# Kernel tuning notes

Hardware: AMD Instinct MI355X
Metric: run time of the kernel (lower is better)

The kernel has to match this reference:

```python
import jax, jax.numpy as jnp
import numpy as np

N, B, F = 204800, 4096, 256

def setup_inputs() -> dict:
    key = jax.random.key(0)
    ks = jax.random.split(key, 8)
    s = 1.0 / np.sqrt(F)
    return {
        'node_feats': jax.random.normal(ks[0], (N, F), jnp.float32),
        'g_feats': jax.random.normal(ks[1], (B, F), jnp.float32),
        'segment_ids': jnp.sort(jax.random.randint(ks[2], (N,), 0, B, jnp.int32)),
        'W_logit': jax.random.normal(ks[3], (1, 2 * F), jnp.float32) * (1.0 / np.sqrt(2 * F)),
        'b_logit': jnp.zeros((1,), jnp.float32),
        'W_proj': jax.random.normal(ks[4], (F, F), jnp.float32) * s,
        'b_proj': jnp.zeros((F,), jnp.float32),
        'W_ih': jax.random.normal(ks[5], (3 * F, F), jnp.float32) * s,
        'W_hh': jax.random.normal(ks[6], (3 * F, F), jnp.float32) * s,
        'b_ih': jnp.zeros((3 * F,), jnp.float32),
        'b_hh': jnp.zeros((3 * F,), jnp.float32),
    }

def reference(node_feats, g_feats, segment_ids, W_logit, b_logit, W_proj, b_proj, W_ih, W_hh, b_ih, b_hh):
    num_graphs = g_feats.shape[0]
    # logits: Linear(2F -> 1) on [broadcast(relu(g_feats)), node_feats], then LeakyReLU(0.01)
    ctx_nodes = jax.nn.relu(g_feats)[segment_ids]                      # [N, F]
    z = jnp.concatenate([ctx_nodes, node_feats], axis=1) @ W_logit.T + b_logit  # [N, 1]
    z = jax.nn.leaky_relu(z, negative_slope=0.01)
    # per-graph segment softmax over nodes
    zmax = jax.ops.segment_max(z, segment_ids, num_segments=num_graphs)
    z_exp = jnp.exp(z - zmax[segment_ids])
    denom = jax.ops.segment_sum(z_exp, segment_ids, num_segments=num_graphs)
    a = z_exp / denom[segment_ids]                                     # [N, 1]
    # project nodes (Dropout is identity at eval) and weighted segment sum
    hv = node_feats @ W_proj.T + b_proj                                # [N, F]
    g_repr = jax.ops.segment_sum(a * hv, segment_ids, num_segments=num_graphs)  # [B, F]
    context = jax.nn.elu(g_repr)
    # PyTorch GRUCell: input=context, hidden=g_feats
    gi = context @ W_ih.T + b_ih                                       # [B, 3F]
    gh = g_feats @ W_hh.T + b_hh
    i_r, i_z, i_n = jnp.split(gi, 3, axis=1)
    h_r, h_z, h_n = jnp.split(gh, 3, axis=1)
    r = jax.nn.sigmoid(i_r + h_r)
    zg = jax.nn.sigmoid(i_z + h_z)
    n = jnp.tanh(i_n + r * h_n)
    return (1.0 - zg) * n + zg * g_feats
```

## Files before the change

kernel.cpp:

```cpp
#include <hip/hip_runtime.h>

#define NN 204800
#define BB 4096
#define FF 256

typedef unsigned short u16;
typedef unsigned int u32;
typedef short bf16x8 __attribute__((ext_vector_type(8)));
typedef float f32x4  __attribute__((ext_vector_type(4)));

__device__ __forceinline__ u16 rne_bf16(float f){
    union { u32 v; float f; } t; t.f = f;
    u32 lsb = (t.v >> 16) & 1u;
    t.v += 0x7fffu + lsb;
    return (u16)(t.v >> 16);
}

__global__ void k_prep(const float* __restrict__ gfe, const float* __restrict__ Wp,
                       const float* __restrict__ Wih, const float* __restrict__ Whh,
                       const int* __restrict__ seg, int* __restrict__ start,
                       u16* __restrict__ gfe_b, u16* __restrict__ Wp_b,
                       u16* __restrict__ Wih_b, u16* __restrict__ Whh_b){
    int i = blockIdx.x * 256 + threadIdx.x;
    if (i <= BB){
        int lo = 0, hi = NN;
        while (lo < hi){ int mid = (lo + hi) >> 1; if (seg[mid] < i) lo = mid + 1; else hi = mid; }
        start[i] = lo;
    }
    const int n_gfe = BB * FF;
    const int n_wp  = FF * FF;
    const int n_w3  = 3 * FF * FF;
    int j = i;
    if (j < n_gfe){ gfe_b[j] = rne_bf16(gfe[j]); return; }
    j -= n_gfe;
    if (j < n_wp){ Wp_b[j] = rne_bf16(Wp[j]); return; }
    j -= n_wp;
    if (j < n_w3){ Wih_b[j] = rne_bf16(Wih[j]); return; }
    j -= n_w3;
    if (j < n_w3){ Whh_b[j] = rne_bf16(Whh[j]); return; }
}
#define PREP_TOTAL (BB*FF + FF*FF + 2*3*FF*FF)

__global__ void k_ctx_logit(const float* __restrict__ gfe, const float* __restrict__ Wl,
                            const float* __restrict__ bl, float* __restrict__ c){
    int wave = threadIdx.x >> 6, lane = threadIdx.x & 63;
    int g = blockIdx.x * 4 + wave;
    float4 gv = *(const float4*)(gfe + (size_t)g * FF + lane * 4);
    float4 wv = *(const float4*)(Wl + lane * 4);
    float sum = wv.x * fmaxf(gv.x, 0.f) + wv.y * fmaxf(gv.y, 0.f)
              + wv.z * fmaxf(gv.z, 0.f) + wv.w * fmaxf(gv.w, 0.f);
    #pragma unroll
    for (int o = 32; o; o >>= 1) sum += __shfl_xor(sum, o);
    if (lane == 0) c[g] = sum + bl[0];
}

__global__ void k_node_logit(const float* __restrict__ x, const float* __restrict__ Wl,
                             const float* __restrict__ c, const int* __restrict__ seg,
                             float* __restrict__ z){
    int wave = threadIdx.x >> 6, lane = threadIdx.x & 63;
    int n = blockIdx.x * 4 + wave;
    float4 xv = *(const float4*)(x + (size_t)n * FF + lane * 4);
    float4 wv = *(const float4*)(Wl + FF + lane * 4);
    float sum = xv.x * wv.x + xv.y * wv.y + xv.z * wv.z + xv.w * wv.w;
    #pragma unroll
    for (int o = 32; o; o >>= 1) sum += __shfl_xor(sum, o);
    if (lane == 0){
        float t = c[seg[n]] + sum;
        z[n] = t >= 0.f ? t : 0.01f * t;
    }
}

__global__ void k_stats(const float* __restrict__ z, const int* __restrict__ start,
                        float* __restrict__ m, float* __restrict__ invd){
    int wave = threadIdx.x >> 6, lane = threadIdx.x & 63;
    int g = blockIdx.x * 4 + wave;
    if (g >= BB) return;
    int s0 = start[g], s1 = start[g + 1];
    float mx = -3.4e38f;
    for (int i = s0 + lane; i < s1; i += 64) mx = fmaxf(mx, z[i]);
    #pragma unroll
    for (int o = 32; o; o >>= 1) mx = fmaxf(mx, __shfl_xor(mx, o));
    float d = 0.f;
    for (int i = s0 + lane; i < s1; i += 64) d += expf(z[i] - mx);
    #pragma unroll
    for (int o = 32; o; o >>= 1) d += __shfl_xor(d, o);
    if (lane == 0){
        m[g] = mx;
        invd[g] = (s1 > s0) ? (1.f / d) : 0.f;
    }
}

__global__ void k_wsum(const float* __restrict__ x, const float* __restrict__ z,
                       const int* __restrict__ start, const float* __restrict__ m,
                       const float* __restrict__ invd, u16* __restrict__ s_b){
    int g = blockIdx.x;
    int t = threadIdx.x;
    int s0 = start[g], s1 = start[g + 1];
    float mg = m[g], iv = invd[g];
    float acc = 0.f;
    for (int n = s0; n < s1; n++){
        float w = expf(z[n] - mg);
        acc += w * x[(size_t)n * FF + t];
    }
    s_b[(size_t)g * FF + t] = rne_bf16(acc * iv);
}

__global__ __launch_bounds__(256) void k_proj_mfma(
        const u16* __restrict__ s_b, const u16* __restrict__ Wp_b,
        const float* __restrict__ bp, const int* __restrict__ gate,
        u16* __restrict__ ctx_b){
    int tid = threadIdx.x;
    int w = tid >> 6, l = tid & 63;
    int mn = l & 15, q = l >> 4;
    int m0 = blockIdx.x * 64 + w * 16;
    int f0 = blockIdx.y * 64;
    f32x4 acc[4] = {};
    const u16* arow = s_b + (size_t)(m0 + mn) * FF + q * 8;
    #pragma unroll
    for (int kb = 0; kb < 8; kb++){
        bf16x8 a = *(const bf16x8*)(arow + kb * 32);
        #pragma unroll
        for (int c = 0; c < 4; c++){
            bf16x8 b = *(const bf16x8*)(Wp_b + (size_t)(f0 + c * 16 + mn) * FF + kb * 32 + q * 8);
            acc[c] = __builtin_amdgcn_mfma_f32_16x16x32_bf16(a, b, acc[c], 0, 0, 0);
        }
    }
    #pragma unroll
    for (int c = 0; c < 4; c++){
        int f = f0 + c * 16 + mn;
        float bias = bp[f];
        #pragma unroll
        for (int r = 0; r < 4; r++){
            int g = m0 + q * 4 + r;
            float bs = (gate[g + 1] > gate[g]) ? 1.f : 0.f;
            float v = acc[c][r] + bs * bias;
            v = v > 0.f ? v : expm1f(v);
            ctx_b[(size_t)g * FF + f] = rne_bf16(v);
        }
    }
}

__global__ __launch_bounds__(256) void k_gru_mfma(
        const u16* __restrict__ ctx_b, const u16* __restrict__ gfe_b,
        const u16* __restrict__ Wih_b, const u16* __restrict__ Whh_b,
        const float* __restrict__ bih, const float* __restrict__ bhh,
        const float* __restrict__ gfe, float* __restrict__ out){
    int tid = threadIdx.x;
    int w = tid >> 6, l = tid & 63;
    int mn = l & 15, q = l >> 4;
    int g0 = blockIdx.x * 64 + w * 16;
    int f0 = blockIdx.y * 64;
    f32x4 ai[3][4] = {};
    f32x4 ah[3][4] = {};
    const u16* ac_row = ctx_b + (size_t)(g0 + mn) * FF + q * 8;
    const u16* ag_row = gfe_b + (size_t)(g0 + mn) * FF + q * 8;
    #pragma unroll
    for (int kb = 0; kb < 8; kb++){
        bf16x8 a_c = *(const bf16x8*)(ac_row + kb * 32);
        bf16x8 a_g = *(const bf16x8*)(ag_row + kb * 32);
        #pragma unroll
        for (int s = 0; s < 3; s++){
            #pragma unroll
            for (int c = 0; c < 4; c++){
                size_t woff = (size_t)(s * FF + f0 + c * 16 + mn) * FF + kb * 32 + q * 8;
                bf16x8 bi = *(const bf16x8*)(Wih_b + woff);
                ai[s][c] = __builtin_amdgcn_mfma_f32_16x16x32_bf16(a_c, bi, ai[s][c], 0, 0, 0);
                bf16x8 bh = *(const bf16x8*)(Whh_b + woff);
                ah[s][c] = __builtin_amdgcn_mfma_f32_16x16x32_bf16(a_g, bh, ah[s][c], 0, 0, 0);
            }
        }
    }
    #pragma unroll
    for (int c = 0; c < 4; c++){
        int f = f0 + c * 16 + mn;
        float bir = bih[f], biz = bih[FF + f], bin_ = bih[2 * FF + f];
        float bhr = bhh[f], bhz = bhh[FF + f], bhn = bhh[2 * FF + f];
        #pragma unroll
        for (int r = 0; r < 4; r++){
            int g = g0 + q * 4 + r;
            float rg = 1.f / (1.f + expf(-(ai[0][c][r] + bir + ah[0][c][r] + bhr)));
            float zg = 1.f / (1.f + expf(-(ai[1][c][r] + biz + ah[1][c][r] + bhz)));
            float ng = tanhf(ai[2][c][r] + bin_ + rg * (ah[2][c][r] + bhn));
            float h = gfe[(size_t)g * FF + f];
            out[(size_t)g * FF + f] = (1.f - zg) * ng + zg * h;
        }
    }
}

extern "C" void kernel_launch(void* const* d_in, const int* in_sizes, int n_in,
                              void* d_out, int out_size, void* d_ws, size_t ws_size,
                              hipStream_t stream){
    const float* node = (const float*)d_in[0];
    const float* gfe  = (const float*)d_in[1];
    const int*   seg  = (const int*)d_in[2];
    const float* Wl   = (const float*)d_in[3];
    const float* bl   = (const float*)d_in[4];
    const float* Wp   = (const float*)d_in[5];
    const float* bp   = (const float*)d_in[6];
    const float* Wih  = (const float*)d_in[7];
    const float* Whh  = (const float*)d_in[8];
    const float* bih  = (const float*)d_in[9];
    const float* bhh  = (const float*)d_in[10];
    float* out = (float*)d_out;

    char* p = (char*)d_ws;
    auto alloc = [&](size_t bytes)->void*{
        void* r = (void*)p; p += (bytes + 255) & ~(size_t)255; return r;
    };
    int*   start = (int*)  alloc((BB + 1) * sizeof(int));
    float* c     = (float*)alloc(BB * sizeof(float));
    float* z     = (float*)alloc(NN * sizeof(float));
    float* mbuf  = (float*)alloc(BB * sizeof(float));
    float* invd  = (float*)alloc(BB * sizeof(float));
    u16*   s_b   = (u16*)  alloc((size_t)BB * FF * sizeof(u16));
    u16*   ctx_b = (u16*)  alloc((size_t)BB * FF * sizeof(u16));
    u16*   gfe_b = (u16*)  alloc((size_t)BB * FF * sizeof(u16));
    u16*   Wp_b  = (u16*)  alloc((size_t)FF * FF * sizeof(u16));
    u16*   Wih_b = (u16*)  alloc((size_t)3 * FF * FF * sizeof(u16));
    u16*   Whh_b = (u16*)  alloc((size_t)3 * FF * FF * sizeof(u16));

    k_prep<<<(PREP_TOTAL + 255) / 256, 256, 0, stream>>>(gfe, Wp, Wih, Whh, seg, start,
                                                         gfe_b, Wp_b, Wih_b, Whh_b);
    k_ctx_logit<<<BB / 4, 256, 0, stream>>>(gfe, Wl, bl, c);
    k_node_logit<<<NN / 4, 256, 0, stream>>>(node, Wl, c, seg, z);
    k_stats<<<BB / 4, 256, 0, stream>>>(z, start, mbuf, invd);
    k_wsum<<<BB, 256, 0, stream>>>(node, z, start, mbuf, invd, s_b);
    k_proj_mfma<<<dim3(BB / 64, FF / 64), 256, 0, stream>>>(s_b, Wp_b, bp, start, ctx_b);
    k_gru_mfma<<<dim3(BB / 64, FF / 64), 256, 0, stream>>>(ctx_b, gfe_b, Wih_b, Whh_b,
                                                           bih, bhh, gfe, out);
}
```

Baseline: 409.9 us.

## Fuse node logits, segment softmax and weighted sum into one per-graph kernel

Replaces three kernels (node logits, per-segment max/denominator, weighted node sum) with a single kernel that runs one block per graph. Each block computes the node logits and stages up to 64 node rows in shared memory, then does the softmax and the weighted sum from that copy. This avoids a second global read of node_feats, the z/max/invd round trips through global memory, and two kernel launches. In exchange it uses about 66KB of LDS per block, which lowers occupancy. The fixed 512-entry logit buffer silently breaks for graphs with more than 512 nodes. It also renames a loop variable in the MFMA kernels.

Result: faster. 385.1 us (-6.1%).

```diff
diff --git a/kernel.cpp b/kernel.cpp
--- a/kernel.cpp
+++ b/kernel.cpp
@@ -3,6 +3,7 @@
 #define NN 204800
 #define BB 4096
 #define FF 256
+#define CAP 64
 
 typedef unsigned short u16;
 typedef unsigned int u32;
@@ -54,55 +55,71 @@
     if (lane == 0) c[g] = sum + bl[0];
 }
 
-__global__ void k_node_logit(const float* __restrict__ x, const float* __restrict__ Wl,
-                             const float* __restrict__ c, const int* __restrict__ seg,
-                             float* __restrict__ z){
-    int wave = threadIdx.x >> 6, lane = threadIdx.x & 63;
-    int n = blockIdx.x * 4 + wave;
-    float4 xv = *(const float4*)(x + (size_t)n * FF + lane * 4);
+__global__ __launch_bounds__(256) void k_attn(
+        const float* __restrict__ x, const float* __restrict__ Wl,
+        const float* __restrict__ c, const int* __restrict__ start,
+        u16* __restrict__ s_b){
+    __shared__ __align__(16) float xs[CAP][FF];
+    __shared__ float zs[512];
+    __shared__ float red[8];
+    int g = blockIdx.x;
+    int s0 = start[g], cnt = start[g + 1] - s0;
+    int tid = threadIdx.x, wave = tid >> 6, lane = tid & 63;
+    if (cnt == 0){
+        s_b[(size_t)g * FF + tid] = 0;
+        return;
+    }
     float4 wv = *(const float4*)(Wl + FF + lane * 4);
-    float sum = xv.x * wv.x + xv.y * wv.y + xv.z * wv.z + xv.w * wv.w;
-    #pragma unroll
-    for (int o = 32; o; o >>= 1) sum += __shfl_xor(sum, o);
-    if (lane == 0){
-        float t = c[seg[n]] + sum;
-        z[n] = t >= 0.f ? t : 0.01f * t;
-    }
-}
-
-__global__ void k_stats(const float* __restrict__ z, const int* __restrict__ start,
-                        float* __restrict__ m, float* __restrict__ invd){
-    int wave = threadIdx.x >> 6, lane = threadIdx.x & 63;
-    int g = blockIdx.x * 4 + wave;
-    if (g >= BB) return;
-    int s0 = start[g], s1 = start[g + 1];
+    float cg = c[g];
+    int i = wave;
+    for (; i + 4 < cnt; i += 8){
+        float4 xv0 = *(const float4*)(x + (size_t)(s0 + i) * FF + lane * 4);
+        float4 xv1 = *(const float4*)(x + (size_t)(s0 + i + 4) * FF + lane * 4);
+        if (i < CAP) *(float4*)(&xs[i][lane * 4]) = xv0;
+        if (i + 4 < CAP) *(float4*)(&xs[i + 4][lane * 4]) = xv1;
+        float d0 = xv0.x * wv.x + xv0.y * wv.y + xv0.z * wv.z + xv0.w * wv.w;
+        float d1 = xv1.x * wv.x + xv1.y * wv.y + xv1.z * wv.z + xv1.w * wv.w;
+        #pragma unroll
+        for (int o = 32; o; o >>= 1){ d0 += __shfl_xor(d0, o); d1 += __shfl_xor(d1, o); }
+        if (lane == 0){
+            float t0 = cg + d0; zs[i] = t0 >= 0.f ? t0 : 0.01f * t0;
+            float t1 = cg + d1; zs[i + 4] = t1 >= 0.f ? t1 : 0.01f * t1;
+        }
+    }
+    for (; i < cnt; i += 4){
+        float4 xv = *(const float4*)(x + (size_t)(s0 + i) * FF + lane * 4);
+        if (i < CAP) *(float4*)(&xs[i][lane * 4]) = xv;
+        float d = xv.x * wv.x + xv.y * wv.y + xv.z * wv.z + xv.w * wv.w;
+        #pragma unroll
+        for (int o = 32; o; o >>= 1) d += __shfl_xor(d, o);
+        if (lane == 0){
+            float t = cg + d; zs[i] = t >= 0.f ? t : 0.01f * t;
+        }
+    }
+    __syncthreads();
     float mx = -3.4e38f;
-    for (int i = s0 + lane; i < s1; i += 64) mx = fmaxf(mx, z[i]);
+    for (int k = tid; k < cnt; k += 256) mx = fmaxf(mx, zs[k]);
     #pragma unroll
     for (int o = 32; o; o >>= 1) mx = fmaxf(mx, __shfl_xor(mx, o));
-    float d = 0.f;
-    for (int i = s0 + lane; i < s1; i += 64) d += expf(z[i] - mx);
-    #pragma unroll
-    for (int o = 32; o; o >>= 1) d += __shfl_xor(d, o);
-    if (lane == 0){
-        m[g] = mx;
-        invd[g] = (s1 > s0) ? (1.f / d) : 0.f;
-    }
-}
-
-__global__ void k_wsum(const float* __restrict__ x, const float* __restrict__ z,
-                       const int* __restrict__ start, const float* __restrict__ m,
-                       const float* __restrict__ invd, u16* __restrict__ s_b){
-    int g = blockIdx.x;
-    int t = threadIdx.x;
-    int s0 = start[g], s1 = start[g + 1];
-    float mg = m[g], iv = invd[g];
+    if (lane == 0) red[wave] = mx;
+    __syncthreads();
+    mx = fmaxf(fmaxf(red[0], red[1]), fmaxf(red[2], red[3]));
+    float dsum = 0.f;
+    for (int k = tid; k < cnt; k += 256){
+        float e = expf(zs[k] - mx);
+        zs[k] = e;
+        dsum += e;
+    }
+    #pragma unroll
+    for (int o = 32; o; o >>= 1) dsum += __shfl_xor(dsum, o);
+    if (lane == 0) red[4 + wave] = dsum;
+    __syncthreads();
+    float inv = 1.f / (red[4] + red[5] + red[6] + red[7]);
     float acc = 0.f;
-    for (int n = s0; n < s1; n++){
-        float w = expf(z[n] - mg);
-        acc += w * x[(size_t)n * FF + t];
-    }
-    s_b[(size_t)g * FF + t] = rne_bf16(acc * iv);
+    int lim = cnt < CAP ? cnt : CAP;
+    for (int k = 0; k < lim; k++) acc += zs[k] * xs[k][tid];
+    for (int k = CAP; k < cnt; k++) acc += zs[k] * x[(size_t)(s0 + k) * FF + tid];
+    s_b[(size_t)g * FF + tid] = rne_bf16(acc * inv);
 }
 
 __global__ __launch_bounds__(256) void k_proj_mfma(
@@ -120,20 +137,20 @@
     for (int kb = 0; kb < 8; kb++){
         bf16x8 a = *(const bf16x8*)(arow + kb * 32);
         #pragma unroll
-        for (int c = 0; c < 4; c++){
-            bf16x8 b = *(const bf16x8*)(Wp_b + (size_t)(f0 + c * 16 + mn) * FF + kb * 32 + q * 8);
-            acc[c] = __builtin_amdgcn_mfma_f32_16x16x32_bf16(a, b, acc[c], 0, 0, 0);
-        }
-    }
-    #pragma unroll
-    for (int c = 0; c < 4; c++){
-        int f = f0 + c * 16 + mn;
+        for (int cc = 0; cc < 4; cc++){
+            bf16x8 b = *(const bf16x8*)(Wp_b + (size_t)(f0 + cc * 16 + mn) * FF + kb * 32 + q * 8);
+            acc[cc] = __builtin_amdgcn_mfma_f32_16x16x32_bf16(a, b, acc[cc], 0, 0, 0);
+        }
+    }
+    #pragma unroll
+    for (int cc = 0; cc < 4; cc++){
+        int f = f0 + cc * 16 + mn;
         float bias = bp[f];
         #pragma unroll
         for (int r = 0; r < 4; r++){
             int g = m0 + q * 4 + r;
             float bs = (gate[g + 1] > gate[g]) ? 1.f : 0.f;
-            float v = acc[c][r] + bs * bias;
+            float v = acc[cc][r] + bs * bias;
             v = v > 0.f ? v : expm1f(v);
             ctx_b[(size_t)g * FF + f] = rne_bf16(v);
         }
@@ -161,26 +178,26 @@
         #pragma unroll
         for (int s = 0; s < 3; s++){
             #pragma unroll
-            for (int c = 0; c < 4; c++){
-                size_t woff = (size_t)(s * FF + f0 + c * 16 + mn) * FF + kb * 32 + q * 8;
+            for (int cc = 0; cc < 4; cc++){
+                size_t woff = (size_t)(s * FF + f0 + cc * 16 + mn) * FF + kb * 32 + q * 8;
                 bf16x8 bi = *(const bf16x8*)(Wih_b + woff);
-                ai[s][c] = __builtin_amdgcn_mfma_f32_16x16x32_bf16(a_c, bi, ai[s][c], 0, 0, 0);
+                ai[s][cc] = __builtin_amdgcn_mfma_f32_16x16x32_bf16(a_c, bi, ai[s][cc], 0, 0, 0);
                 bf16x8 bh = *(const bf16x8*)(Whh_b + woff);
-                ah[s][c] = __builtin_amdgcn_mfma_f32_16x16x32_bf16(a_g, bh, ah[s][c], 0, 0, 0);
+                ah[s][cc] = __builtin_amdgcn_mfma_f32_16x16x32_bf16(a_g, bh, ah[s][cc], 0, 0, 0);
             }
         }
     }
     #pragma unroll
-    for (int c = 0; c < 4; c++){
-        int f = f0 + c * 16 + mn;
+    for (int cc = 0; cc < 4; cc++){
+        int f = f0 + cc * 16 + mn;
         float bir = bih[f], biz = bih[FF + f], bin_ = bih[2 * FF + f];
         float bhr = bhh[f], bhz = bhh[FF + f], bhn = bhh[2 * FF + f];
         #pragma unroll
         for (int r = 0; r < 4; r++){
             int g = g0 + q * 4 + r;
-            float rg = 1.f / (1.f + expf(-(ai[0][c][r] + bir + ah[0][c][r] + bhr)));
-            float zg = 1.f / (1.f + expf(-(ai[1][c][r] + biz + ah[1][c][r] + bhz)));
-            float ng = tanhf(ai[2][c][r] + bin_ + rg * (ah[2][c][r] + bhn));
+            float rg = 1.f / (1.f + expf(-(ai[0][cc][r] + bir + ah[0][cc][r] + bhr)));
+            float zg = 1.f / (1.f + expf(-(ai[1][cc][r] + biz + ah[1][cc][r] + bhz)));
+            float ng = tanhf(ai[2][cc][r] + bin_ + rg * (ah[2][cc][r] + bhn));
             float h = gfe[(size_t)g * FF + f];
             out[(size_t)g * FF + f] = (1.f - zg) * ng + zg * h;
         }
@@ -209,9 +226,6 @@
     };
     int*   start = (int*)  alloc((BB + 1) * sizeof(int));
     float* c     = (float*)alloc(BB * sizeof(float));
-    float* z     = (float*)alloc(NN * sizeof(float));
-    float* mbuf  = (float*)alloc(BB * sizeof(float));
-    float* invd  = (float*)alloc(BB * sizeof(float));
     u16*   s_b   = (u16*)  alloc((size_t)BB * FF * sizeof(u16));
     u16*   ctx_b = (u16*)  alloc((size_t)BB * FF * sizeof(u16));
     u16*   gfe_b = (u16*)  alloc((size_t)BB * FF * sizeof(u16));
@@ -222,9 +236,7 @@
     k_prep<<<(PREP_TOTAL + 255) / 256, 256, 0, stream>>>(gfe, Wp, Wih, Whh, seg, start,
                                                          gfe_b, Wp_b, Wih_b, Whh_b);
     k_ctx_logit<<<BB / 4, 256, 0, stream>>>(gfe, Wl, bl, c);
-    k_node_logit<<<NN / 4, 256, 0, stream>>>(node, Wl, c, seg, z);
-    k_stats<<<BB / 4, 256, 0, stream>>>(z, start, mbuf, invd);
-    k_wsum<<<BB, 256, 0, stream>>>(node, z, start, mbuf, invd, s_b);
+    k_attn<<<BB, 256, 0, stream>>>(node, Wl, c, start, s_b);
     k_proj_mfma<<<dim3(BB / 64, FF / 64), 256, 0, stream>>>(s_b, Wp_b, bp, start, ctx_b);
     k_gru_mfma<<<dim3(BB / 64, FF / 64), 256, 0, stream>>>(ctx_b, gfe_b, Wih_b, Whh_b,
                                                            bih, bhh, gfe, out);
```
